# Kernel optimization log

Measured on AMD Instinct MI355X. Metric: run time of the kernel, lower is better.

## Reference

```python
import jax, jax.numpy as jnp
import numpy as np

GENES = 20000   # input gene nodes (depth 0)
LEVEL = 10000   # nodes per subsequent depth level
STEPS = 7       # depth propagation steps
DEG = 16        # in-degree per dst node
N = GENES + STEPS * LEVEL          # 90000 total nodes
EPS = LEVEL * DEG                  # 160000 edges per step
E = STEPS * EPS                    # 1120000 total edges
B = 256
C = 2


def setup_inputs() -> dict:
    key = jax.random.key(0)
    k0, k1, k2 = jax.random.split(key, 3)
    X = jax.random.normal(k0, (B, GENES), jnp.float32)
    gene_map = jnp.arange(GENES, dtype=jnp.int32)

    rng = np.random.default_rng(0)
    src_list, dstu_list = [], []
    for k in range(STEPS):
        lo = 0 if k == 0 else GENES + (k - 1) * LEVEL
        hi = GENES if k == 0 else lo + LEVEL
        src_list.append(rng.integers(lo, hi, size=EPS))
        dstu_list.append(np.arange(GENES + k * LEVEL, GENES + (k + 1) * LEVEL))
    src = jnp.asarray(np.stack(src_list), dtype=jnp.int32)          # [STEPS, EPS]
    dst_unique = jnp.asarray(np.stack(dstu_list), dtype=jnp.int32)  # [STEPS, LEVEL]
    dst_pos = jnp.tile(jnp.repeat(jnp.arange(LEVEL, dtype=jnp.int32), DEG)[None, :], (STEPS, 1))
    eid = jnp.arange(E, dtype=jnp.int32).reshape(STEPS, EPS)
    root_ids = dst_unique[-1]

    edge_weight = jax.random.normal(k1, (E,), jnp.float32) * 0.01
    node_bias = jnp.zeros((N,), jnp.float32)
    head_W = jax.random.normal(k2, (LEVEL, C), jnp.float32) * (1.0 / np.sqrt(LEVEL))
    head_b = jnp.zeros((C,), jnp.float32)

    return dict(X=X, edge_weight=edge_weight, node_bias=node_bias,
                head_W=head_W, head_b=head_b, gene_map=gene_map,
                src=src, dst_pos=dst_pos, dst_unique=dst_unique,
                eid=eid, root_ids=root_ids)


def reference(X, edge_weight, node_bias, head_W, head_b,
              gene_map, src, dst_pos, dst_unique, eid, root_ids):
    # dropout is identity (eval mode / p=0)
    b = X.shape[0]
    h = jnp.zeros((b, N), X.dtype).at[:, gene_map].set(X)
    for k in range(src.shape[0]):  # fixed small number of depth steps
        w = edge_weight[eid[k]]                                   # [EPS]
        msg = h[:, src[k]] * w[None, :]                           # gather + scale [B, EPS]
        agg = jnp.zeros((b, dst_unique.shape[1]), h.dtype).at[:, dst_pos[k]].add(msg)
        h_dst = jnp.tanh(agg + node_bias[dst_unique[k]][None, :])  # [B, LEVEL]
        h = h.at[:, dst_unique[k]].set(h_dst)
    roots = h[:, root_ids]                                        # [B, LEVEL]
    return roots @ head_W + head_b
```

## Files before the change

kernel.cpp:

```cpp
#include <hip/hip_runtime.h>
#include <math.h>

#define GENES 20000
#define LEVEL 10000
#define STEPS 7
#define DEG   16
#define EPSZ  (LEVEL * DEG)
#define CCOLS 32
#define NCHUNK 8
#define NDG   313
#define SBLK  157
#define NGT   625

typedef unsigned short bf4 __attribute__((ext_vector_type(4)));
typedef unsigned short bf8 __attribute__((ext_vector_type(8)));

__device__ inline float bf2f(unsigned short u) {
    union { unsigned u; float f; } c; c.u = ((unsigned)u) << 16; return c.f;
}
__device__ inline unsigned short f2bf(float x) {
    union { float f; unsigned u; } c; c.f = x;
    return (unsigned short)((c.u + 0x7fffu + ((c.u >> 16) & 1u)) >> 16);
}

__global__ __launch_bounds__(256) void transpose_k(const float* __restrict__ X,
                                                   const int*   __restrict__ gene_map,
                                                   unsigned short* __restrict__ XT) {
    __shared__ float tile[32][33];
    const int chunk = blockIdx.x;
    const int lo = threadIdx.x & 31, r = threadIdx.x >> 5;
    unsigned short* XTp = XT + (size_t)chunk * GENES * CCOLS;
    for (int i = 0; i < 4; ++i) {
        const int gt = blockIdx.y * 4 + i;
        if (gt >= NGT) break;
        const int g0 = gt * 32;
        if (i) __syncthreads();
#pragma unroll
        for (int j = 0; j < 4; ++j) {
            const int b = r + j * 8;
            tile[b][lo] = X[(size_t)(chunk * CCOLS + b) * GENES + g0 + lo];
        }
        __syncthreads();
#pragma unroll
        for (int j = 0; j < 4; ++j) {
            const int gr   = r + j * 8;
            const int node = gene_map[g0 + gr];
            XTp[(size_t)node * CCOLS + lo] = f2bf(tile[lo][gr]);
        }
    }
}

__global__ __launch_bounds__(256) void step_k(const unsigned short* __restrict__ hprev,
                                              unsigned short*       __restrict__ hcur,
                                              const int*   __restrict__ src_k,
                                              const float* __restrict__ w_k,
                                              const float* __restrict__ node_bias,
                                              const int*   __restrict__ dstu_k,
                                              int src_base, int prev_rows) {
    const int bid   = blockIdx.x;
    const int chunk = bid & 7;
    const int cb    = bid >> 3;
    const int wave  = threadIdx.x >> 6;
    const int lane  = threadIdx.x & 63;
    const int q     = lane >> 2;
    const int c8    = (lane & 3) * 8;

    const int dest = cb * 64 + wave * 16 + q;
    if (dest >= LEVEL) return;

    const unsigned short* prev = hprev + (size_t)chunk * prev_rows * CCOLS;
    unsigned short*       curp = hcur + (size_t)chunk * LEVEL * CCOLS;

    const int be = dest * DEG;
    const int4   s0 = *reinterpret_cast<const int4*>  (src_k + be);
    const int4   s1 = *reinterpret_cast<const int4*>  (src_k + be + 4);
    const int4   s2 = *reinterpret_cast<const int4*>  (src_k + be + 8);
    const int4   s3 = *reinterpret_cast<const int4*>  (src_k + be + 12);
    const float4 w0 = *reinterpret_cast<const float4*>(w_k + be);
    const float4 w1 = *reinterpret_cast<const float4*>(w_k + be + 4);
    const float4 w2 = *reinterpret_cast<const float4*>(w_k + be + 8);
    const float4 w3 = *reinterpret_cast<const float4*>(w_k + be + 12);

    float a0 = 0.f, a1 = 0.f, a2 = 0.f, a3 = 0.f, a4 = 0.f, a5 = 0.f, a6 = 0.f, a7 = 0.f;
#define ACC(sv, wv) { const int idx = (sv) - src_base;                                      \
    const bf8 v = *reinterpret_cast<const bf8*>(prev + (size_t)idx * CCOLS + c8);           \
    a0 = fmaf(bf2f(v[0]), (wv), a0); a1 = fmaf(bf2f(v[1]), (wv), a1);                       \
    a2 = fmaf(bf2f(v[2]), (wv), a2); a3 = fmaf(bf2f(v[3]), (wv), a3);                       \
    a4 = fmaf(bf2f(v[4]), (wv), a4); a5 = fmaf(bf2f(v[5]), (wv), a5);                       \
    a6 = fmaf(bf2f(v[6]), (wv), a6); a7 = fmaf(bf2f(v[7]), (wv), a7); }
    ACC(s0.x, w0.x) ACC(s0.y, w0.y) ACC(s0.z, w0.z) ACC(s0.w, w0.w)
    ACC(s1.x, w1.x) ACC(s1.y, w1.y) ACC(s1.z, w1.z) ACC(s1.w, w1.w)
    ACC(s2.x, w2.x) ACC(s2.y, w2.y) ACC(s2.z, w2.z) ACC(s2.w, w2.w)
    ACC(s3.x, w3.x) ACC(s3.y, w3.y) ACC(s3.z, w3.z) ACC(s3.w, w3.w)
#undef ACC
    const float bz = node_bias[dstu_k[dest]];
    bf8 o;
    o[0] = f2bf(tanhf(a0 + bz));
    o[1] = f2bf(tanhf(a1 + bz));
    o[2] = f2bf(tanhf(a2 + bz));
    o[3] = f2bf(tanhf(a3 + bz));
    o[4] = f2bf(tanhf(a4 + bz));
    o[5] = f2bf(tanhf(a5 + bz));
    o[6] = f2bf(tanhf(a6 + bz));
    o[7] = f2bf(tanhf(a7 + bz));
    *reinterpret_cast<bf8*>(curp + (size_t)dest * CCOLS + c8) = o;
}

__global__ __launch_bounds__(256) void step7_head_k(const unsigned short* __restrict__ hprev,
                                                    const int*   __restrict__ src_k,
                                                    const float* __restrict__ w_k,
                                                    const float* __restrict__ node_bias,
                                                    const int*   __restrict__ dstu_k,
                                                    const float* __restrict__ head_W,
                                                    float*       __restrict__ part,
                                                    int src_base) {
    const int bid   = blockIdx.x;
    const int chunk = bid & 7;
    const int cb    = bid >> 3;
    const int wave  = threadIdx.x >> 6;
    const int lane  = threadIdx.x & 63;
    const int g     = lane >> 3;
    const int colh  = (lane & 7) * 4;

    const unsigned short* prev = hprev + (size_t)chunk * LEVEL * CCOLS;

    float h0 = 0.f, h1 = 0.f, h2 = 0.f, h3 = 0.f, h4 = 0.f, h5 = 0.f, h6 = 0.f, h7 = 0.f;

#pragma unroll
    for (int jj = 0; jj < 2; ++jj) {
        const int dg = cb + jj * SBLK;
        if (dg >= NDG) continue;
        const int dest = dg * 32 + wave * 8 + g;
        if (dest >= LEVEL) continue;

        const int be = dest * DEG;
        const int4   s0 = *reinterpret_cast<const int4*>  (src_k + be);
        const int4   s1 = *reinterpret_cast<const int4*>  (src_k + be + 4);
        const int4   s2 = *reinterpret_cast<const int4*>  (src_k + be + 8);
        const int4   s3 = *reinterpret_cast<const int4*>  (src_k + be + 12);
        const float4 w0 = *reinterpret_cast<const float4*>(w_k + be);
        const float4 w1 = *reinterpret_cast<const float4*>(w_k + be + 4);
        const float4 w2 = *reinterpret_cast<const float4*>(w_k + be + 8);
        const float4 w3 = *reinterpret_cast<const float4*>(w_k + be + 12);

        float a0 = 0.f, a1 = 0.f, a2 = 0.f, a3 = 0.f;
#define ACC(sv, wv) { const int idx = (sv) - src_base;                                      \
    const bf4 v = *reinterpret_cast<const bf4*>(prev + (size_t)idx * CCOLS + colh);         \
    a0 = fmaf(bf2f(v[0]), (wv), a0); a1 = fmaf(bf2f(v[1]), (wv), a1);                       \
    a2 = fmaf(bf2f(v[2]), (wv), a2); a3 = fmaf(bf2f(v[3]), (wv), a3); }
        ACC(s0.x, w0.x) ACC(s0.y, w0.y) ACC(s0.z, w0.z) ACC(s0.w, w0.w)
        ACC(s1.x, w1.x) ACC(s1.y, w1.y) ACC(s1.z, w1.z) ACC(s1.w, w1.w)
        ACC(s2.x, w2.x) ACC(s2.y, w2.y) ACC(s2.z, w2.z) ACC(s2.w, w2.w)
        ACC(s3.x, w3.x) ACC(s3.y, w3.y) ACC(s3.z, w3.z) ACC(s3.w, w3.w)
#undef ACC
        const float bz = node_bias[dstu_k[dest]];
        const float o0 = tanhf(a0 + bz);
        const float o1 = tanhf(a1 + bz);
        const float o2 = tanhf(a2 + bz);
        const float o3 = tanhf(a3 + bz);
        const float2 wv = *reinterpret_cast<const float2*>(head_W + dest * 2);
        h0 = fmaf(o0, wv.x, h0); h1 = fmaf(o0, wv.y, h1);
        h2 = fmaf(o1, wv.x, h2); h3 = fmaf(o1, wv.y, h3);
        h4 = fmaf(o2, wv.x, h4); h5 = fmaf(o2, wv.y, h5);
        h6 = fmaf(o3, wv.x, h6); h7 = fmaf(o3, wv.y, h7);
    }

#pragma unroll
    for (int m = 8; m < 64; m <<= 1) {
        h0 += __shfl_xor(h0, m); h1 += __shfl_xor(h1, m);
        h2 += __shfl_xor(h2, m); h3 += __shfl_xor(h3, m);
        h4 += __shfl_xor(h4, m); h5 += __shfl_xor(h5, m);
        h6 += __shfl_xor(h6, m); h7 += __shfl_xor(h7, m);
    }
    __shared__ float red[4][8][8];
    if (lane < 8) {
        red[wave][lane][0] = h0; red[wave][lane][1] = h1;
        red[wave][lane][2] = h2; red[wave][lane][3] = h3;
        red[wave][lane][4] = h4; red[wave][lane][5] = h5;
        red[wave][lane][6] = h6; red[wave][lane][7] = h7;
    }
    __syncthreads();
    if (threadIdx.x < 64) {
        const int l8 = threadIdx.x >> 3, v = threadIdx.x & 7;
        const float s = red[0][l8][v] + red[1][l8][v] + red[2][l8][v] + red[3][l8][v];
        part[((size_t)chunk * SBLK + cb) * 64 + threadIdx.x] = s;
    }
}

__global__ __launch_bounds__(64) void head_final_k(const float* __restrict__ part,
                                                   const float* __restrict__ head_b,
                                                   float*       __restrict__ out) {
    const int chunk = blockIdx.x;
    const int t     = threadIdx.x;
    float acc = head_b[t & 1];
    for (int q = 0; q < SBLK; ++q)
        acc += part[((size_t)chunk * SBLK + q) * 64 + t];
    out[chunk * 64 + t] = acc;
}

extern "C" void kernel_launch(void* const* d_in, const int* in_sizes, int n_in,
                              void* d_out, int out_size, void* d_ws, size_t ws_size,
                              hipStream_t stream) {
    const float* X           = (const float*)d_in[0];
    const float* edge_weight = (const float*)d_in[1];
    const float* node_bias   = (const float*)d_in[2];
    const float* head_W      = (const float*)d_in[3];
    const float* head_b      = (const float*)d_in[4];
    const int*   gene_map    = (const int*)  d_in[5];
    const int*   src         = (const int*)  d_in[6];
    const int*   dst_unique  = (const int*)  d_in[8];
    float* out = (float*)d_out;

    char* ws = (char*)d_ws;
    unsigned short* XT   = (unsigned short*)(ws);
    unsigned short* lvlA = (unsigned short*)(ws + 10240000);
    unsigned short* lvlB = (unsigned short*)(ws + 15360000);
    float*          part = (float*)         (ws + 20480000);

    transpose_k<<<dim3(NCHUNK, 157), 256, 0, stream>>>(X, gene_map, XT);

    unsigned short* bufs[2] = {lvlA, lvlB};
    for (int k = 0; k < STEPS - 1; ++k) {
        const unsigned short* hprev = (k == 0) ? XT : bufs[(k - 1) & 1];
        const int prevrows = (k == 0) ? GENES : LEVEL;
        const int srcbase  = (k == 0) ? 0 : GENES + (k - 1) * LEVEL;
        step_k<<<SBLK * NCHUNK, 256, 0, stream>>>(hprev, bufs[k & 1],
                                                  src + (size_t)k * EPSZ,
                                                  edge_weight + (size_t)k * EPSZ,
                                                  node_bias,
                                                  dst_unique + (size_t)k * LEVEL,
                                                  srcbase, prevrows);
    }

    {
        const int k = STEPS - 1;
        const unsigned short* hprev = bufs[(k - 1) & 1];
        const int srcbase = GENES + (k - 1) * LEVEL;
        step7_head_k<<<SBLK * NCHUNK, 256, 0, stream>>>(hprev,
                                                        src + (size_t)k * EPSZ,
                                                        edge_weight + (size_t)k * EPSZ,
                                                        node_bias,
                                                        dst_unique + (size_t)k * LEVEL,
                                                        head_W, part, srcbase);
        head_final_k<<<NCHUNK, 64, 0, stream>>>(part, head_b, out);
    }
    (void)in_sizes; (void)n_in; (void)out_size; (void)ws_size;
}
```

Measured before the change: 93.48 us.

## Stage edge src/weights in LDS and restructure head reduction via shared tile

Both step kernels now cooperatively load each block's contiguous slice of src indices and edge weights into shared memory with coalesced int4/float4 loads, then read per-destination rows from LDS. The final step+head kernel is restructured to process 64 destinations per block with 8-wide bf16 gathers (matching step_k), writes tanh outputs to an LDS tile, and does the head matmul reduction through shared memory instead of wave shuffles. This trades strided per-thread global loads for a block barrier and extra LDS traffic.

```diff
diff --git a/kernel.cpp b/kernel.cpp
--- a/kernel.cpp
+++ b/kernel.cpp
@@ -8,11 +8,10 @@
 #define EPSZ  (LEVEL * DEG)
 #define CCOLS 32
 #define NCHUNK 8
-#define NDG   313
 #define SBLK  157
 #define NGT   625
-
-typedef unsigned short bf4 __attribute__((ext_vector_type(4)));
+#define MSTRIDE 18
+
 typedef unsigned short bf8 __attribute__((ext_vector_type(8)));
 
 __device__ inline float bf2f(unsigned short u) {
@@ -60,26 +59,41 @@
     const int bid   = blockIdx.x;
     const int chunk = bid & 7;
     const int cb    = bid >> 3;
-    const int wave  = threadIdx.x >> 6;
-    const int lane  = threadIdx.x & 63;
-    const int q     = lane >> 2;
-    const int c8    = (lane & 3) * 8;
-
-    const int dest = cb * 64 + wave * 16 + q;
+    const int tid   = threadIdx.x;
+
+    __shared__ int   s_src[64 * MSTRIDE];
+    __shared__ float s_w  [64 * MSTRIDE];
+
+    {
+        const int m4 = cb * 256 + tid;
+        if (m4 < EPSZ / 4) {
+            const int4   sv = reinterpret_cast<const int4*>(src_k)[m4];
+            const float4 wv = reinterpret_cast<const float4*>(w_k)[m4];
+            const int j = tid >> 2, i = (tid & 3) * 4;
+            *reinterpret_cast<int4*>  (&s_src[j * MSTRIDE + i]) = sv;
+            *reinterpret_cast<float4*>(&s_w  [j * MSTRIDE + i]) = wv;
+        }
+    }
+    __syncthreads();
+
+    const int wave = tid >> 6, lane = tid & 63;
+    const int q    = lane >> 2;
+    const int c8   = (lane & 3) * 8;
+    const int j    = wave * 16 + q;
+    const int dest = cb * 64 + j;
     if (dest >= LEVEL) return;
 
     const unsigned short* prev = hprev + (size_t)chunk * prev_rows * CCOLS;
     unsigned short*       curp = hcur + (size_t)chunk * LEVEL * CCOLS;
 
-    const int be = dest * DEG;
-    const int4   s0 = *reinterpret_cast<const int4*>  (src_k + be);
-    const int4   s1 = *reinterpret_cast<const int4*>  (src_k + be + 4);
-    const int4   s2 = *reinterpret_cast<const int4*>  (src_k + be + 8);
-    const int4   s3 = *reinterpret_cast<const int4*>  (src_k + be + 12);
-    const float4 w0 = *reinterpret_cast<const float4*>(w_k + be);
-    const float4 w1 = *reinterpret_cast<const float4*>(w_k + be + 4);
-    const float4 w2 = *reinterpret_cast<const float4*>(w_k + be + 8);
-    const float4 w3 = *reinterpret_cast<const float4*>(w_k + be + 12);
+    const int4   s0 = *reinterpret_cast<const int4*>  (&s_src[j * MSTRIDE + 0]);
+    const int4   s1 = *reinterpret_cast<const int4*>  (&s_src[j * MSTRIDE + 4]);
+    const int4   s2 = *reinterpret_cast<const int4*>  (&s_src[j * MSTRIDE + 8]);
+    const int4   s3 = *reinterpret_cast<const int4*>  (&s_src[j * MSTRIDE + 12]);
+    const float4 w0 = *reinterpret_cast<const float4*>(&s_w  [j * MSTRIDE + 0]);
+    const float4 w1 = *reinterpret_cast<const float4*>(&s_w  [j * MSTRIDE + 4]);
+    const float4 w2 = *reinterpret_cast<const float4*>(&s_w  [j * MSTRIDE + 8]);
+    const float4 w3 = *reinterpret_cast<const float4*>(&s_w  [j * MSTRIDE + 12]);
 
     float a0 = 0.f, a1 = 0.f, a2 = 0.f, a3 = 0.f, a4 = 0.f, a5 = 0.f, a6 = 0.f, a7 = 0.f;
 #define ACC(sv, wv) { const int idx = (sv) - src_base;                                      \
@@ -117,73 +131,93 @@
     const int bid   = blockIdx.x;
     const int chunk = bid & 7;
     const int cb    = bid >> 3;
-    const int wave  = threadIdx.x >> 6;
-    const int lane  = threadIdx.x & 63;
-    const int g     = lane >> 3;
-    const int colh  = (lane & 7) * 4;
+    const int tid   = threadIdx.x;
+
+    __shared__ int   s_src[64 * MSTRIDE];
+    __shared__ float s_w  [64 * MSTRIDE];
+    __shared__ float o_tile[64][33];
+    __shared__ float s_W2[64][2];
+    __shared__ float red[8][64];
+
+    {
+        const int m4 = cb * 256 + tid;
+        if (m4 < EPSZ / 4) {
+            const int4   sv = reinterpret_cast<const int4*>(src_k)[m4];
+            const float4 wv = reinterpret_cast<const float4*>(w_k)[m4];
+            const int j = tid >> 2, i = (tid & 3) * 4;
+            *reinterpret_cast<int4*>  (&s_src[j * MSTRIDE + i]) = sv;
+            *reinterpret_cast<float4*>(&s_w  [j * MSTRIDE + i]) = wv;
+        }
+    }
+    if (tid < 32) {
+        const int f4 = cb * 32 + tid;
+        float4 wv = make_float4(0.f, 0.f, 0.f, 0.f);
+        if (f4 < (LEVEL * 2) / 4) wv = reinterpret_cast<const float4*>(head_W)[f4];
+        s_W2[tid * 2 + 0][0] = wv.x; s_W2[tid * 2 + 0][1] = wv.y;
+        s_W2[tid * 2 + 1][0] = wv.z; s_W2[tid * 2 + 1][1] = wv.w;
+    }
+    __syncthreads();
+
+    const int wave = tid >> 6, lane = tid & 63;
+    const int q    = lane >> 2;
+    const int c8   = (lane & 3) * 8;
+    const int j    = wave * 16 + q;
+    const int dest = cb * 64 + j;
 
     const unsigned short* prev = hprev + (size_t)chunk * LEVEL * CCOLS;
 
-    float h0 = 0.f, h1 = 0.f, h2 = 0.f, h3 = 0.f, h4 = 0.f, h5 = 0.f, h6 = 0.f, h7 = 0.f;
-
-#pragma unroll
-    for (int jj = 0; jj < 2; ++jj) {
-        const int dg = cb + jj * SBLK;
-        if (dg >= NDG) continue;
-        const int dest = dg * 32 + wave * 8 + g;
-        if (dest >= LEVEL) continue;
-
-        const int be = dest * DEG;
-        const int4   s0 = *reinterpret_cast<const int4*>  (src_k + be);
-        const int4   s1 = *reinterpret_cast<const int4*>  (src_k + be + 4);
-        const int4   s2 = *reinterpret_cast<const int4*>  (src_k + be + 8);
-        const int4   s3 = *reinterpret_cast<const int4*>  (src_k + be + 12);
-        const float4 w0 = *reinterpret_cast<const float4*>(w_k + be);
-        const float4 w1 = *reinterpret_cast<const float4*>(w_k + be + 4);
-        const float4 w2 = *reinterpret_cast<const float4*>(w_k + be + 8);
-        const float4 w3 = *reinterpret_cast<const float4*>(w_k + be + 12);
-
-        float a0 = 0.f, a1 = 0.f, a2 = 0.f, a3 = 0.f;
+    float o0 = 0.f, o1 = 0.f, o2 = 0.f, o3 = 0.f, o4 = 0.f, o5 = 0.f, o6 = 0.f, o7 = 0.f;
+    if (dest < LEVEL) {
+        const int4   s0 = *reinterpret_cast<const int4*>  (&s_src[j * MSTRIDE + 0]);
+        const int4   s1 = *reinterpret_cast<const int4*>  (&s_src[j * MSTRIDE + 4]);
+        const int4   s2 = *reinterpret_cast<const int4*>  (&s_src[j * MSTRIDE + 8]);
+        const int4   s3 = *reinterpret_cast<const int4*>  (&s_src[j * MSTRIDE + 12]);
+        const float4 w0 = *reinterpret_cast<const float4*>(&s_w  [j * MSTRIDE + 0]);
+        const float4 w1 = *reinterpret_cast<const float4*>(&s_w  [j * MSTRIDE + 4]);
+        const float4 w2 = *reinterpret_cast<const float4*>(&s_w  [j * MSTRIDE + 8]);
+        const float4 w3 = *reinterpret_cast<const float4*>(&s_w  [j * MSTRIDE + 12]);
+
+        float a0 = 0.f, a1 = 0.f, a2 = 0.f, a3 = 0.f, a4 = 0.f, a5 = 0.f, a6 = 0.f, a7 = 0.f;
 #define ACC(sv, wv) { const int idx = (sv) - src_base;                                      \
-    const bf4 v = *reinterpret_cast<const bf4*>(prev + (size_t)idx * CCOLS + colh);         \
+    const bf8 v = *reinterpret_cast<const bf8*>(prev + (size_t)idx * CCOLS + c8);           \
     a0 = fmaf(bf2f(v[0]), (wv), a0); a1 = fmaf(bf2f(v[1]), (wv), a1);                       \
-    a2 = fmaf(bf2f(v[2]), (wv), a2); a3 = fmaf(bf2f(v[3]), (wv), a3); }
+    a2 = fmaf(bf2f(v[2]), (wv), a2); a3 = fmaf(bf2f(v[3]), (wv), a3);                       \
+    a4 = fmaf(bf2f(v[4]), (wv), a4); a5 = fmaf(bf2f(v[5]), (wv), a5);                       \
+    a6 = fmaf(bf2f(v[6]), (wv), a6); a7 = fmaf(bf2f(v[7]), (wv), a7); }
         ACC(s0.x, w0.x) ACC(s0.y, w0.y) ACC(s0.z, w0.z) ACC(s0.w, w0.w)
         ACC(s1.x, w1.x) ACC(s1.y, w1.y) ACC(s1.z, w1.z) ACC(s1.w, w1.w)
         ACC(s2.x, w2.x) ACC(s2.y, w2.y) ACC(s2.z, w2.z) ACC(s2.w, w2.w)
         ACC(s3.x, w3.x) ACC(s3.y, w3.y) ACC(s3.z, w3.z) ACC(s3.w, w3.w)
 #undef ACC
         const float bz = node_bias[dstu_k[dest]];
-        const float o0 = tanhf(a0 + bz);
-        const float o1 = tanhf(a1 + bz);
-        const float o2 = tanhf(a2 + bz);
-        const float o3 = tanhf(a3 + bz);
-        const float2 wv = *reinterpret_cast<const float2*>(head_W + dest * 2);
-        h0 = fmaf(o0, wv.x, h0); h1 = fmaf(o0, wv.y, h1);
-        h2 = fmaf(o1, wv.x, h2); h3 = fmaf(o1, wv.y, h3);
-        h4 = fmaf(o2, wv.x, h4); h5 = fmaf(o2, wv.y, h5);
-        h6 = fmaf(o3, wv.x, h6); h7 = fmaf(o3, wv.y, h7);
-    }
-
-#pragma unroll
-    for (int m = 8; m < 64; m <<= 1) {
-        h0 += __shfl_xor(h0, m); h1 += __shfl_xor(h1, m);
-        h2 += __shfl_xor(h2, m); h3 += __shfl_xor(h3, m);
-        h4 += __shfl_xor(h4, m); h5 += __shfl_xor(h5, m);
-        h6 += __shfl_xor(h6, m); h7 += __shfl_xor(h7, m);
-    }
-    __shared__ float red[4][8][8];
-    if (lane < 8) {
-        red[wave][lane][0] = h0; red[wave][lane][1] = h1;
-        red[wave][lane][2] = h2; red[wave][lane][3] = h3;
-        red[wave][lane][4] = h4; red[wave][lane][5] = h5;
-        red[wave][lane][6] = h6; red[wave][lane][7] = h7;
-    }
-    __syncthreads();
-    if (threadIdx.x < 64) {
-        const int l8 = threadIdx.x >> 3, v = threadIdx.x & 7;
-        const float s = red[0][l8][v] + red[1][l8][v] + red[2][l8][v] + red[3][l8][v];
-        part[((size_t)chunk * SBLK + cb) * 64 + threadIdx.x] = s;
+        o0 = tanhf(a0 + bz); o1 = tanhf(a1 + bz); o2 = tanhf(a2 + bz); o3 = tanhf(a3 + bz);
+        o4 = tanhf(a4 + bz); o5 = tanhf(a5 + bz); o6 = tanhf(a6 + bz); o7 = tanhf(a7 + bz);
+    }
+    o_tile[j][c8 + 0] = o0; o_tile[j][c8 + 1] = o1;
+    o_tile[j][c8 + 2] = o2; o_tile[j][c8 + 3] = o3;
+    o_tile[j][c8 + 4] = o4; o_tile[j][c8 + 5] = o5;
+    o_tile[j][c8 + 6] = o6; o_tile[j][c8 + 7] = o7;
+    __syncthreads();
+
+    {
+        const int col = tid & 31, slot = tid >> 5;
+        float a0 = 0.f, a1 = 0.f;
+#pragma unroll
+        for (int e = 0; e < 8; ++e) {
+            const int jj = slot * 8 + e;
+            const float v = o_tile[jj][col];
+            a0 = fmaf(v, s_W2[jj][0], a0);
+            a1 = fmaf(v, s_W2[jj][1], a1);
+        }
+        red[slot][col * 2 + 0] = a0;
+        red[slot][col * 2 + 1] = a1;
+    }
+    __syncthreads();
+    if (tid < 64) {
+        float s = 0.f;
+#pragma unroll
+        for (int p = 0; p < 8; ++p) s += red[p][tid];
+        part[((size_t)chunk * SBLK + cb) * 64 + tid] = s;
     }
 }
 
```

Measured after the change: 91.68 us. No clear change (-1.9%).
